# Kernel optimization log

Hardware: AMD Instinct MI355X
Metric: run time of the kernel (lower is better)

## Reference

```python
import jax, jax.numpy as jnp
import numpy as np

INPUT_SIZE = 512
HIDDEN_SIZE = 512
BATCH = 128
SEQ_LEN = 512


def setup_inputs() -> dict:
    key = jax.random.key(0)
    k_xs, k_wih, k_whh, k_b, k_bn = jax.random.split(key, 5)
    lim = 1.0 / np.sqrt(HIDDEN_SIZE)  # equinox GRUCell init: U(-1/sqrt(H), 1/sqrt(H))
    xs = jax.random.normal(k_xs, (BATCH, SEQ_LEN, INPUT_SIZE), dtype=jnp.float32)
    weight_ih = jax.random.uniform(k_wih, (3 * HIDDEN_SIZE, INPUT_SIZE), minval=-lim, maxval=lim, dtype=jnp.float32)
    weight_hh = jax.random.uniform(k_whh, (3 * HIDDEN_SIZE, HIDDEN_SIZE), minval=-lim, maxval=lim, dtype=jnp.float32)
    bias = jax.random.uniform(k_b, (3 * HIDDEN_SIZE,), minval=-lim, maxval=lim, dtype=jnp.float32)
    bias_n = jax.random.uniform(k_bn, (HIDDEN_SIZE,), minval=-lim, maxval=lim, dtype=jnp.float32)
    return {"xs": xs, "weight_ih": weight_ih, "weight_hh": weight_hh, "bias": bias, "bias_n": bias_n}


def _gru_scan(xs, weight_ih, weight_hh, bias, bias_n):
    # xs: [B, T, I]. Precompute all input-side gates in one big GEMM: [B, T, 3H]
    igates_all = jnp.einsum('bti,gi->btg', xs, weight_ih) + bias
    B = xs.shape[0]
    H = weight_hh.shape[1]

    def step(h, ig_t):  # h: [B, H], ig_t: [B, 3H]
        hg = h @ weight_hh.T  # [B, 3H]
        ir, iz, in_ = jnp.split(ig_t, 3, axis=-1)
        hr, hz, hn = jnp.split(hg, 3, axis=-1)
        r = jax.nn.sigmoid(ir + hr)
        z = jax.nn.sigmoid(iz + hz)
        n = jnp.tanh(in_ + r * (hn + bias_n))
        h_new = n + z * (h - n)  # equinox GRUCell: new + inp*(hidden - new)
        return h_new, None

    init = jnp.zeros((B, H), dtype=xs.dtype)
    final_state, _ = jax.lax.scan(step, init, jnp.swapaxes(igates_all, 0, 1))  # scan over T
    return final_state  # [B, H]


def reference(xs, weight_ih, weight_hh, bias, bias_n):
    return _gru_scan(xs, weight_ih, weight_hh, bias, bias_n)
```

## Files before the change

kernel.cpp:

```cpp
#include <hip/hip_runtime.h>
#include <hip/hip_bf16.h>
#include <stdint.h>


static constexpr int INPUT = 512;
static constexpr int HID   = 512;
static constexpr int NB    = 128;
static constexpr int TLEN  = 512;
static constexpr int BGRPS = 8;
static constexpr int UGRPS = 32;

typedef __attribute__((ext_vector_type(4))) float f32x4;
typedef __attribute__((ext_vector_type(8))) short s16x8;

static __device__ __forceinline__ unsigned short f2bf(float f) {
  unsigned u = __builtin_bit_cast(unsigned, f);
  u += 0x7FFFu + ((u >> 16) & 1u);
  return (unsigned short)(u >> 16);
}

static __device__ __forceinline__ s16x8 cvt8(const float* p) {
  f32x4 a = *(const f32x4*)p;
  f32x4 b = *(const f32x4*)(p + 4);
  s16x8 r;
  r[0] = (short)f2bf(a[0]); r[1] = (short)f2bf(a[1]);
  r[2] = (short)f2bf(a[2]); r[3] = (short)f2bf(a[3]);
  r[4] = (short)f2bf(b[0]); r[5] = (short)f2bf(b[1]);
  r[6] = (short)f2bf(b[2]); r[7] = (short)f2bf(b[3]);
  return r;
}

__global__ __launch_bounds__(192, 2) void gru_fused(
    const float* __restrict__ xs, const float* __restrict__ wih,
    const float* __restrict__ whh, const float* __restrict__ bias,
    const float* __restrict__ bias_n, float* __restrict__ out,
    unsigned short* __restrict__ hbuf, unsigned int* __restrict__ flags)
{
  const int wg   = blockIdx.x;
  const int bgrp = wg & 7;
  const int ugrp = wg >> 3;
  const int b0   = bgrp * 16;
  const int u0   = ugrp * 16;
  const int tid  = threadIdx.x;
  const int g    = tid >> 6;
  const int lane = tid & 63;
  const int ln   = lane & 15;
  const int kg   = lane >> 4;

  const int rowW = g * HID + u0 + ln;
  s16x8 wa[16], wb[16];
#pragma unroll
  for (int ks = 0; ks < 16; ++ks) {
    const int k = ks * 32 + kg * 8;
    wa[ks] = cvt8(wih + (size_t)rowW * INPUT + k);
    wb[ks] = cvt8(whh + (size_t)rowW * HID + k);
  }
  const float bv = bias[rowW];
  const float bn = bias_n[u0 + ln];

  const float* xrow = xs + (size_t)(b0 + ln) * TLEN * INPUT + kg * 8;
  const int hoff = (b0 + ln) * HID + kg * 8;

  __shared__ float xch[2][4][16][16];

  float hold[4] = {0.f, 0.f, 0.f, 0.f};

  f32x4 acc_a = {bv, bv, bv, bv};
#pragma unroll
  for (int ks = 0; ks < 16; ++ks) {
    s16x8 xa = cvt8(xrow + ks * 32);
    acc_a = __builtin_amdgcn_mfma_f32_16x16x32_bf16(xa, wa[ks], acc_a, 0, 0, 0);
  }

  for (int t = 0; t < TLEN; ++t) {
    if (t > 0) {
      const unsigned* fp = &flags[bgrp * UGRPS + (lane & 31)];
      unsigned fv;
      do {
        fv = __hip_atomic_load(fp, __ATOMIC_RELAXED, __HIP_MEMORY_SCOPE_AGENT);
      } while (~__ballot(fv >= (unsigned)t));
      __builtin_amdgcn_sched_barrier(0);
    }

    const unsigned long long* hb =
        (const unsigned long long*)(hbuf + (size_t)(t & 1) * (NB * HID) + hoff);
    unsigned long long q0[16], q1[16];
#pragma unroll
    for (int ks = 0; ks < 16; ++ks) {
      q0[ks] = __hip_atomic_load(hb + ks * 8,     __ATOMIC_RELAXED, __HIP_MEMORY_SCOPE_AGENT);
      q1[ks] = __hip_atomic_load(hb + ks * 8 + 1, __ATOMIC_RELAXED, __HIP_MEMORY_SCOPE_AGENT);
    }

    f32x4 acc_b0 = {0.f, 0.f, 0.f, 0.f}, acc_b1 = {0.f, 0.f, 0.f, 0.f};
#pragma unroll
    for (int ks = 0; ks < 16; ks += 2) {
      union { unsigned long long q[2]; s16x8 s; } ua, ub;
      ua.q[0] = q0[ks];     ua.q[1] = q1[ks];
      ub.q[0] = q0[ks + 1]; ub.q[1] = q1[ks + 1];
      acc_b0 = __builtin_amdgcn_mfma_f32_16x16x32_bf16(ua.s, wb[ks],     acc_b0, 0, 0, 0);
      acc_b1 = __builtin_amdgcn_mfma_f32_16x16x32_bf16(ub.s, wb[ks + 1], acc_b1, 0, 0, 0);
    }
    f32x4 acc_b = acc_b0 + acc_b1;

    float (*xc)[16][16] = xch[t & 1];
    if (g == 0)      { f32x4 s = acc_a + acc_b; *(f32x4*)&xc[0][ln][kg * 4] = s; }
    else if (g == 1) { f32x4 s = acc_a + acc_b; *(f32x4*)&xc[1][ln][kg * 4] = s; }
    else             { *(f32x4*)&xc[2][ln][kg * 4] = acc_a;
                       *(f32x4*)&xc[3][ln][kg * 4] = acc_b; }
    __syncthreads();
    f32x4 Sr  = *(const f32x4*)&xc[0][ln][kg * 4];
    f32x4 Sz  = *(const f32x4*)&xc[1][ln][kg * 4];
    f32x4 Snx = *(const f32x4*)&xc[2][ln][kg * 4];
    f32x4 Snh = *(const f32x4*)&xc[3][ln][kg * 4];

    float hnew[4];
#pragma unroll
    for (int i = 0; i < 4; ++i) {
      float r = 1.f / (1.f + __expf(-Sr[i]));
      float z = 1.f / (1.f + __expf(-Sz[i]));
      float pre = Snx[i] + r * (Snh[i] + bn);
      float e = __expf(2.f * pre);
      float n = 1.f - 2.f / (e + 1.f);
      hnew[i] = n + z * (hold[i] - n);
      hold[i] = hnew[i];
    }

    if (t == TLEN - 1) {
      if (g == 0) {
#pragma unroll
        for (int i = 0; i < 4; ++i)
          out[(size_t)(b0 + kg * 4 + i) * HID + u0 + ln] = hnew[i];
      }
    } else {
      if (g == 0) {
        unsigned short* hbn = hbuf + (size_t)((t + 1) & 1) * (NB * HID);
#pragma unroll
        for (int i = 0; i < 4; ++i) {
          int v  = (int)f2bf(hnew[i]);
          int o1 = __shfl_xor(v, 1);
          unsigned int p = (unsigned int)(v & 0xffff) | ((unsigned int)(o1 & 0xffff) << 16);
          unsigned int o2 = (unsigned int)__shfl_xor((int)p, 2);
          if ((ln & 3) == 0) {
            unsigned long long q = (unsigned long long)p | ((unsigned long long)o2 << 32);
            __hip_atomic_store(
                (unsigned long long*)(hbn + (size_t)(b0 + kg * 4 + i) * HID + u0 + ln),
                q, __ATOMIC_RELAXED, __HIP_MEMORY_SCOPE_AGENT);
          }
        }
        asm volatile("s_waitcnt vmcnt(0)" ::: "memory");
        if (tid == 0)
          __hip_atomic_store(&flags[bgrp * UGRPS + ugrp], (unsigned)(t + 1),
                             __ATOMIC_RELAXED, __HIP_MEMORY_SCOPE_AGENT);
      }

      acc_a = (f32x4){bv, bv, bv, bv};
      const float* xp = xrow + (size_t)(t + 1) * INPUT;
#pragma unroll
      for (int ks = 0; ks < 16; ++ks) {
        s16x8 xa = cvt8(xp + ks * 32);
        acc_a = __builtin_amdgcn_mfma_f32_16x16x32_bf16(xa, wa[ks], acc_a, 0, 0, 0);
      }
    }
  }
}

extern "C" void kernel_launch(void* const* d_in, const int* in_sizes, int n_in,
                              void* d_out, int out_size, void* d_ws, size_t ws_size,
                              hipStream_t stream) {
  const float* xs     = (const float*)d_in[0];
  const float* wih    = (const float*)d_in[1];
  const float* whh    = (const float*)d_in[2];
  const float* bias   = (const float*)d_in[3];
  const float* bias_n = (const float*)d_in[4];
  float* out = (float*)d_out;

  const size_t hbuf_bytes = (size_t)2 * NB * HID * sizeof(unsigned short);
  const size_t flg_bytes  = (size_t)BGRPS * UGRPS * sizeof(unsigned int);
  unsigned short* hbuf  = (unsigned short*)d_ws;
  unsigned int*   flags = (unsigned int*)((char*)d_ws + hbuf_bytes);

  hipMemsetAsync(d_ws, 0, hbuf_bytes + flg_bytes, stream);

  gru_fused<<<dim3(BGRPS * UGRPS), dim3(192), 0, stream>>>(
      xs, wih, whh, bias, bias_n, out, hbuf, flags);
}
```

Before: 3.553 ms.

## Use XCD-local L2-coherent loads when a batch group shares one XCD

At startup every workgroup records its XCC_ID, then checks whether all 32 workgroups of its batch group sit on the same XCD. If they do, the per-step flag polling and hidden-state exchange use plain sc0 loads and non-atomic stores, which are coherent at the XCD-local L2, in place of device-scope atomics, and the hidden-state read becomes sixteen dwordx4 loads. The bf16 conversion in cvt8 also switches to the packed hardware instruction, which changes rounding only if it differs from the old manual round-to-nearest-even. Correctness depends on the dispatch placement and on L2 coherence assumptions, and the fast path only runs when the groups land on one XCD.

```diff
diff --git a/kernel.cpp b/kernel.cpp
--- a/kernel.cpp
+++ b/kernel.cpp
@@ -12,6 +12,7 @@
 
 typedef __attribute__((ext_vector_type(4))) float f32x4;
 typedef __attribute__((ext_vector_type(8))) short s16x8;
+typedef __attribute__((ext_vector_type(4))) int   i32x4;
 
 static __device__ __forceinline__ unsigned short f2bf(float f) {
   unsigned u = __builtin_bit_cast(unsigned, f);
@@ -22,19 +23,22 @@
 static __device__ __forceinline__ s16x8 cvt8(const float* p) {
   f32x4 a = *(const f32x4*)p;
   f32x4 b = *(const f32x4*)(p + 4);
-  s16x8 r;
-  r[0] = (short)f2bf(a[0]); r[1] = (short)f2bf(a[1]);
-  r[2] = (short)f2bf(a[2]); r[3] = (short)f2bf(a[3]);
-  r[4] = (short)f2bf(b[0]); r[5] = (short)f2bf(b[1]);
-  r[6] = (short)f2bf(b[2]); r[7] = (short)f2bf(b[3]);
-  return r;
+  unsigned r0, r1, r2, r3;
+  asm("v_cvt_pk_bf16_f32 %0, %1, %2" : "=v"(r0) : "v"(a[0]), "v"(a[1]));
+  asm("v_cvt_pk_bf16_f32 %0, %1, %2" : "=v"(r1) : "v"(a[2]), "v"(a[3]));
+  asm("v_cvt_pk_bf16_f32 %0, %1, %2" : "=v"(r2) : "v"(b[0]), "v"(b[1]));
+  asm("v_cvt_pk_bf16_f32 %0, %1, %2" : "=v"(r3) : "v"(b[2]), "v"(b[3]));
+  union { unsigned u[4]; s16x8 s; } r;
+  r.u[0] = r0; r.u[1] = r1; r.u[2] = r2; r.u[3] = r3;
+  return r.s;
 }
 
 __global__ __launch_bounds__(192, 2) void gru_fused(
     const float* __restrict__ xs, const float* __restrict__ wih,
     const float* __restrict__ whh, const float* __restrict__ bias,
     const float* __restrict__ bias_n, float* __restrict__ out,
-    unsigned short* __restrict__ hbuf, unsigned int* __restrict__ flags)
+    unsigned short* __restrict__ hbuf, unsigned int* __restrict__ flags,
+    unsigned int* __restrict__ xcdmap)
 {
   const int wg   = blockIdx.x;
   const int bgrp = wg & 7;
@@ -47,6 +51,12 @@
   const int ln   = lane & 15;
   const int kg   = lane >> 4;
 
+  if (tid == 0) {
+    unsigned x;
+    asm volatile("s_getreg_b32 %0, hwreg(HW_REG_XCC_ID)" : "=s"(x));
+    __hip_atomic_store(&xcdmap[wg], x | 0x100u, __ATOMIC_RELAXED, __HIP_MEMORY_SCOPE_AGENT);
+  }
+
   const int rowW = g * HID + u0 + ln;
   s16x8 wa[16], wb[16];
 #pragma unroll
@@ -58,10 +68,22 @@
   const float bv = bias[rowW];
   const float bn = bias_n[u0 + ln];
 
+  __shared__ int fast_sh;
+  __shared__ float xch[2][4][16][16];
+  if (tid < 32) {
+    unsigned v;
+    do {
+      v = __hip_atomic_load(&xcdmap[bgrp + 8 * tid], __ATOMIC_RELAXED, __HIP_MEMORY_SCOPE_AGENT);
+    } while (v == 0);
+    unsigned v0 = (unsigned)__shfl((int)v, 0);
+    unsigned long long bal = __ballot(v == v0);
+    if (tid == 0) fast_sh = ((bal & 0xFFFFFFFFull) == 0xFFFFFFFFull) ? 1 : 0;
+  }
+  __syncthreads();
+  const bool fast = (fast_sh != 0);
+
   const float* xrow = xs + (size_t)(b0 + ln) * TLEN * INPUT + kg * 8;
   const int hoff = (b0 + ln) * HID + kg * 8;
-
-  __shared__ float xch[2][4][16][16];
 
   float hold[4] = {0.f, 0.f, 0.f, 0.f};
 
@@ -76,29 +98,71 @@
     if (t > 0) {
       const unsigned* fp = &flags[bgrp * UGRPS + (lane & 31)];
       unsigned fv;
-      do {
-        fv = __hip_atomic_load(fp, __ATOMIC_RELAXED, __HIP_MEMORY_SCOPE_AGENT);
-      } while (~__ballot(fv >= (unsigned)t));
+      if (fast) {
+        do {
+          asm volatile("global_load_dword %0, %1, off sc0\n\t"
+                       "s_waitcnt vmcnt(0)"
+                       : "=&v"(fv) : "v"(fp) : "memory");
+        } while (~__ballot(fv >= (unsigned)t));
+      } else {
+        do {
+          fv = __hip_atomic_load(fp, __ATOMIC_RELAXED, __HIP_MEMORY_SCOPE_AGENT);
+        } while (~__ballot(fv >= (unsigned)t));
+      }
       __builtin_amdgcn_sched_barrier(0);
     }
 
-    const unsigned long long* hb =
-        (const unsigned long long*)(hbuf + (size_t)(t & 1) * (NB * HID) + hoff);
-    unsigned long long q0[16], q1[16];
-#pragma unroll
-    for (int ks = 0; ks < 16; ++ks) {
-      q0[ks] = __hip_atomic_load(hb + ks * 8,     __ATOMIC_RELAXED, __HIP_MEMORY_SCOPE_AGENT);
-      q1[ks] = __hip_atomic_load(hb + ks * 8 + 1, __ATOMIC_RELAXED, __HIP_MEMORY_SCOPE_AGENT);
+    s16x8 hu[16];
+    if (fast) {
+      const char* hb = (const char*)(hbuf + (size_t)(t & 1) * (NB * HID) + hoff);
+      i32x4 h0,h1,h2,h3,h4,h5,h6,h7,h8,h9,h10,h11,h12,h13,h14,h15;
+      asm volatile(
+        "global_load_dwordx4 %0,  %16, off sc0\n\t"
+        "global_load_dwordx4 %1,  %16, off offset:64 sc0\n\t"
+        "global_load_dwordx4 %2,  %16, off offset:128 sc0\n\t"
+        "global_load_dwordx4 %3,  %16, off offset:192 sc0\n\t"
+        "global_load_dwordx4 %4,  %16, off offset:256 sc0\n\t"
+        "global_load_dwordx4 %5,  %16, off offset:320 sc0\n\t"
+        "global_load_dwordx4 %6,  %16, off offset:384 sc0\n\t"
+        "global_load_dwordx4 %7,  %16, off offset:448 sc0\n\t"
+        "global_load_dwordx4 %8,  %16, off offset:512 sc0\n\t"
+        "global_load_dwordx4 %9,  %16, off offset:576 sc0\n\t"
+        "global_load_dwordx4 %10, %16, off offset:640 sc0\n\t"
+        "global_load_dwordx4 %11, %16, off offset:704 sc0\n\t"
+        "global_load_dwordx4 %12, %16, off offset:768 sc0\n\t"
+        "global_load_dwordx4 %13, %16, off offset:832 sc0\n\t"
+        "global_load_dwordx4 %14, %16, off offset:896 sc0\n\t"
+        "global_load_dwordx4 %15, %16, off offset:960 sc0"
+        : "=&v"(h0),"=&v"(h1),"=&v"(h2),"=&v"(h3),"=&v"(h4),"=&v"(h5),"=&v"(h6),"=&v"(h7),
+          "=&v"(h8),"=&v"(h9),"=&v"(h10),"=&v"(h11),"=&v"(h12),"=&v"(h13),"=&v"(h14),"=&v"(h15)
+        : "v"(hb) : "memory");
+      asm volatile("s_waitcnt vmcnt(0)" ::: "memory");
+      __builtin_amdgcn_sched_barrier(0);
+      hu[0]=__builtin_bit_cast(s16x8,h0);   hu[1]=__builtin_bit_cast(s16x8,h1);
+      hu[2]=__builtin_bit_cast(s16x8,h2);   hu[3]=__builtin_bit_cast(s16x8,h3);
+      hu[4]=__builtin_bit_cast(s16x8,h4);   hu[5]=__builtin_bit_cast(s16x8,h5);
+      hu[6]=__builtin_bit_cast(s16x8,h6);   hu[7]=__builtin_bit_cast(s16x8,h7);
+      hu[8]=__builtin_bit_cast(s16x8,h8);   hu[9]=__builtin_bit_cast(s16x8,h9);
+      hu[10]=__builtin_bit_cast(s16x8,h10); hu[11]=__builtin_bit_cast(s16x8,h11);
+      hu[12]=__builtin_bit_cast(s16x8,h12); hu[13]=__builtin_bit_cast(s16x8,h13);
+      hu[14]=__builtin_bit_cast(s16x8,h14); hu[15]=__builtin_bit_cast(s16x8,h15);
+    } else {
+      const unsigned long long* hb =
+          (const unsigned long long*)(hbuf + (size_t)(t & 1) * (NB * HID) + hoff);
+#pragma unroll
+      for (int ks = 0; ks < 16; ++ks) {
+        union { unsigned long long q[2]; s16x8 s; } u;
+        u.q[0] = __hip_atomic_load(hb + ks * 8,     __ATOMIC_RELAXED, __HIP_MEMORY_SCOPE_AGENT);
+        u.q[1] = __hip_atomic_load(hb + ks * 8 + 1, __ATOMIC_RELAXED, __HIP_MEMORY_SCOPE_AGENT);
+        hu[ks] = u.s;
+      }
     }
 
     f32x4 acc_b0 = {0.f, 0.f, 0.f, 0.f}, acc_b1 = {0.f, 0.f, 0.f, 0.f};
 #pragma unroll
     for (int ks = 0; ks < 16; ks += 2) {
-      union { unsigned long long q[2]; s16x8 s; } ua, ub;
-      ua.q[0] = q0[ks];     ua.q[1] = q1[ks];
-      ub.q[0] = q0[ks + 1]; ub.q[1] = q1[ks + 1];
-      acc_b0 = __builtin_amdgcn_mfma_f32_16x16x32_bf16(ua.s, wb[ks],     acc_b0, 0, 0, 0);
-      acc_b1 = __builtin_amdgcn_mfma_f32_16x16x32_bf16(ub.s, wb[ks + 1], acc_b1, 0, 0, 0);
+      acc_b0 = __builtin_amdgcn_mfma_f32_16x16x32_bf16(hu[ks],     wb[ks],     acc_b0, 0, 0, 0);
+      acc_b1 = __builtin_amdgcn_mfma_f32_16x16x32_bf16(hu[ks + 1], wb[ks + 1], acc_b1, 0, 0, 0);
     }
     f32x4 acc_b = acc_b0 + acc_b1;
 
@@ -142,15 +206,19 @@
           unsigned int o2 = (unsigned int)__shfl_xor((int)p, 2);
           if ((ln & 3) == 0) {
             unsigned long long q = (unsigned long long)p | ((unsigned long long)o2 << 32);
-            __hip_atomic_store(
-                (unsigned long long*)(hbn + (size_t)(b0 + kg * 4 + i) * HID + u0 + ln),
-                q, __ATOMIC_RELAXED, __HIP_MEMORY_SCOPE_AGENT);
+            unsigned long long* qa =
+                (unsigned long long*)(hbn + (size_t)(b0 + kg * 4 + i) * HID + u0 + ln);
+            if (fast) *qa = q;
+            else __hip_atomic_store(qa, q, __ATOMIC_RELAXED, __HIP_MEMORY_SCOPE_AGENT);
           }
         }
         asm volatile("s_waitcnt vmcnt(0)" ::: "memory");
-        if (tid == 0)
-          __hip_atomic_store(&flags[bgrp * UGRPS + ugrp], (unsigned)(t + 1),
-                             __ATOMIC_RELAXED, __HIP_MEMORY_SCOPE_AGENT);
+        if (tid == 0) {
+          unsigned* fw = &flags[bgrp * UGRPS + ugrp];
+          if (fast) *(volatile unsigned*)fw = (unsigned)(t + 1);
+          else __hip_atomic_store(fw, (unsigned)(t + 1),
+                                  __ATOMIC_RELAXED, __HIP_MEMORY_SCOPE_AGENT);
+        }
       }
 
       acc_a = (f32x4){bv, bv, bv, bv};
@@ -176,11 +244,13 @@
 
   const size_t hbuf_bytes = (size_t)2 * NB * HID * sizeof(unsigned short);
   const size_t flg_bytes  = (size_t)BGRPS * UGRPS * sizeof(unsigned int);
+  const size_t xcd_bytes  = (size_t)BGRPS * UGRPS * sizeof(unsigned int);
   unsigned short* hbuf  = (unsigned short*)d_ws;
   unsigned int*   flags = (unsigned int*)((char*)d_ws + hbuf_bytes);
-
-  hipMemsetAsync(d_ws, 0, hbuf_bytes + flg_bytes, stream);
+  unsigned int*   xcdm  = (unsigned int*)((char*)d_ws + hbuf_bytes + flg_bytes);
+
+  hipMemsetAsync(d_ws, 0, hbuf_bytes + flg_bytes + xcd_bytes, stream);
 
   gru_fused<<<dim3(BGRPS * UGRPS), dim3(192), 0, stream>>>(
-      xs, wih, whh, bias, bias_n, out, hbuf, flags);
-}
+      xs, wih, whh, bias, bias_n, out, hbuf, flags, xcdm);
+}
```

Result: slower. 4.285 ms (+20.6%).

## Stage x rows through swizzled LDS ring buffer with cooperative prefetch

Applied to the files above, without the earlier changes.

Replaces each wave's redundant per-timestep global load and bf16 conversion of x with a cooperative load. All 192 threads fetch the 16x512 x tile for step t+2 into registers, convert it to bf16 and store it into a triple-buffered, XOR-swizzled LDS ring. Each wave then reads its x fragments from LDS for the input-gate MFMAs. The input-gate MFMA now runs inside the timestep after the flag wait, not after publishing h. The change also uses the hardware v_cvt_pk_bf16_f32 packed conversion instead of manual rounding. This cuts global x traffic per workgroup (three waves previously loaded the same x) and hides load latency. The cost is 48KB of LDS, which may hurt the 2-blocks-per-CU occupancy, and input-gate work placed on the critical path after the wait.

```diff
diff --git a/kernel.cpp b/kernel.cpp
--- a/kernel.cpp
+++ b/kernel.cpp
@@ -9,6 +9,8 @@
 static constexpr int TLEN  = 512;
 static constexpr int BGRPS = 8;
 static constexpr int UGRPS = 32;
+static constexpr int PD    = 2;
+static constexpr int NBUF  = 3;
 
 typedef __attribute__((ext_vector_type(4))) float f32x4;
 typedef __attribute__((ext_vector_type(8))) short s16x8;
@@ -22,12 +24,28 @@
 static __device__ __forceinline__ s16x8 cvt8(const float* p) {
   f32x4 a = *(const f32x4*)p;
   f32x4 b = *(const f32x4*)(p + 4);
-  s16x8 r;
-  r[0] = (short)f2bf(a[0]); r[1] = (short)f2bf(a[1]);
-  r[2] = (short)f2bf(a[2]); r[3] = (short)f2bf(a[3]);
-  r[4] = (short)f2bf(b[0]); r[5] = (short)f2bf(b[1]);
-  r[6] = (short)f2bf(b[2]); r[7] = (short)f2bf(b[3]);
-  return r;
+  unsigned r0, r1, r2, r3;
+  asm("v_cvt_pk_bf16_f32 %0, %1, %2" : "=v"(r0) : "v"(a[0]), "v"(a[1]));
+  asm("v_cvt_pk_bf16_f32 %0, %1, %2" : "=v"(r1) : "v"(a[2]), "v"(a[3]));
+  asm("v_cvt_pk_bf16_f32 %0, %1, %2" : "=v"(r2) : "v"(b[0]), "v"(b[1]));
+  asm("v_cvt_pk_bf16_f32 %0, %1, %2" : "=v"(r3) : "v"(b[2]), "v"(b[3]));
+  union { unsigned u[4]; s16x8 s; } r;
+  r.u[0] = r0; r.u[1] = r1; r.u[2] = r2; r.u[3] = r3;
+  return r.s;
+}
+
+static __device__ __forceinline__ int tile_byte(int idx) {
+  int rw = idx >> 7, c = idx & 127;
+  return rw * 1024 + ((c * 8) ^ ((rw & 7) << 4));
+}
+
+static __device__ __forceinline__ void st_tile(char* xtb, int idx, f32x4 v) {
+  unsigned lo, hi;
+  asm("v_cvt_pk_bf16_f32 %0, %1, %2" : "=v"(lo) : "v"(v[0]), "v"(v[1]));
+  asm("v_cvt_pk_bf16_f32 %0, %1, %2" : "=v"(hi) : "v"(v[2]), "v"(v[3]));
+  union { unsigned u[2]; unsigned long long q; } r;
+  r.u[0] = lo; r.u[1] = hi;
+  *(unsigned long long*)(xtb + tile_byte(idx)) = r.q;
 }
 
 __global__ __launch_bounds__(192, 2) void gru_fused(
@@ -47,6 +65,9 @@
   const int ln   = lane & 15;
   const int kg   = lane >> 4;
 
+  __shared__ unsigned short xt[NBUF][16 * 512];
+  __shared__ float xch[2][4][16][16];
+
   const int rowW = g * HID + u0 + ln;
   s16x8 wa[16], wb[16];
 #pragma unroll
@@ -58,19 +79,25 @@
   const float bv = bias[rowW];
   const float bn = bias_n[u0 + ln];
 
-  const float* xrow = xs + (size_t)(b0 + ln) * TLEN * INPUT + kg * 8;
+  const size_t xbase = (size_t)b0 * TLEN * INPUT;
   const int hoff = (b0 + ln) * HID + kg * 8;
 
-  __shared__ float xch[2][4][16][16];
+  for (int p = 0; p < PD; ++p) {
+    char* xtb = (char*)&xt[p][0];
+#pragma unroll
+    for (int k = 0; k < 11; ++k) {
+      int idx = tid + k * 192;
+      if (idx < 2048) {
+        int rw = idx >> 7, c = idx & 127;
+        f32x4 v = *(const f32x4*)(xs + xbase + (size_t)rw * TLEN * INPUT +
+                                  (size_t)p * INPUT + c * 4);
+        st_tile(xtb, idx, v);
+      }
+    }
+  }
+  __syncthreads();
 
   float hold[4] = {0.f, 0.f, 0.f, 0.f};
-
-  f32x4 acc_a = {bv, bv, bv, bv};
-#pragma unroll
-  for (int ks = 0; ks < 16; ++ks) {
-    s16x8 xa = cvt8(xrow + ks * 32);
-    acc_a = __builtin_amdgcn_mfma_f32_16x16x32_bf16(xa, wa[ks], acc_a, 0, 0, 0);
-  }
 
   for (int t = 0; t < TLEN; ++t) {
     if (t > 0) {
@@ -91,6 +118,31 @@
       q1[ks] = __hip_atomic_load(hb + ks * 8 + 1, __ATOMIC_RELAXED, __HIP_MEMORY_SCOPE_AGENT);
     }
 
+    f32x4 xr[11];
+    const bool do_stage = (t + PD < TLEN);
+    if (do_stage) {
+#pragma unroll
+      for (int k = 0; k < 11; ++k) {
+        int idx = tid + k * 192;
+        if (idx < 2048) {
+          int rw = idx >> 7, c = idx & 127;
+          xr[k] = *(const f32x4*)(xs + xbase + (size_t)rw * TLEN * INPUT +
+                                  (size_t)(t + PD) * INPUT + c * 4);
+        }
+      }
+    }
+
+    f32x4 acc_a = {bv, bv, bv, bv};
+    {
+      const char* xtb = (const char*)&xt[t % NBUF][0];
+#pragma unroll
+      for (int ks = 0; ks < 16; ++ks) {
+        int byte = ln * 1024 + ((ks * 64 + kg * 16) ^ ((ln & 7) << 4));
+        s16x8 xa = *(const s16x8*)(xtb + byte);
+        acc_a = __builtin_amdgcn_mfma_f32_16x16x32_bf16(xa, wa[ks], acc_a, 0, 0, 0);
+      }
+    }
+
     f32x4 acc_b0 = {0.f, 0.f, 0.f, 0.f}, acc_b1 = {0.f, 0.f, 0.f, 0.f};
 #pragma unroll
     for (int ks = 0; ks < 16; ks += 2) {
@@ -107,7 +159,17 @@
     else if (g == 1) { f32x4 s = acc_a + acc_b; *(f32x4*)&xc[1][ln][kg * 4] = s; }
     else             { *(f32x4*)&xc[2][ln][kg * 4] = acc_a;
                        *(f32x4*)&xc[3][ln][kg * 4] = acc_b; }
+
+    if (do_stage) {
+      char* xtb = (char*)&xt[(t + PD) % NBUF][0];
+#pragma unroll
+      for (int k = 0; k < 11; ++k) {
+        int idx = tid + k * 192;
+        if (idx < 2048) st_tile(xtb, idx, xr[k]);
+      }
+    }
     __syncthreads();
+
     f32x4 Sr  = *(const f32x4*)&xc[0][ln][kg * 4];
     f32x4 Sz  = *(const f32x4*)&xc[1][ln][kg * 4];
     f32x4 Snx = *(const f32x4*)&xc[2][ln][kg * 4];
@@ -152,14 +214,6 @@
           __hip_atomic_store(&flags[bgrp * UGRPS + ugrp], (unsigned)(t + 1),
                              __ATOMIC_RELAXED, __HIP_MEMORY_SCOPE_AGENT);
       }
-
-      acc_a = (f32x4){bv, bv, bv, bv};
-      const float* xp = xrow + (size_t)(t + 1) * INPUT;
-#pragma unroll
-      for (int ks = 0; ks < 16; ++ks) {
-        s16x8 xa = cvt8(xp + ks * 32);
-        acc_a = __builtin_amdgcn_mfma_f32_16x16x32_bf16(xa, wa[ks], acc_a, 0, 0, 0);
-      }
     }
   }
 }
```

Result: slower. 4.912 ms (+38.2%).

## Stage hidden state in LDS via one wave; use packed bf16 convert

Applied to the files above, without the earlier changes.

Only wave 0 now polls the per-step flags and loads the 16x512 bf16 hidden-state tile from global memory into swizzled shared memory. All three waves then read their MFMA operands from LDS after a block barrier. Before, each of the three waves spun on the flags and issued its own global atomic loads. This cuts global traffic and polling by three times, at the cost of an extra __syncthreads and LDS round trip on the critical recurrent path. The f32-to-bf16 conversion also switches to the hardware packed convert instruction instead of manual rounding.

```diff
diff --git a/kernel.cpp b/kernel.cpp
--- a/kernel.cpp
+++ b/kernel.cpp
@@ -22,12 +22,14 @@
 static __device__ __forceinline__ s16x8 cvt8(const float* p) {
   f32x4 a = *(const f32x4*)p;
   f32x4 b = *(const f32x4*)(p + 4);
-  s16x8 r;
-  r[0] = (short)f2bf(a[0]); r[1] = (short)f2bf(a[1]);
-  r[2] = (short)f2bf(a[2]); r[3] = (short)f2bf(a[3]);
-  r[4] = (short)f2bf(b[0]); r[5] = (short)f2bf(b[1]);
-  r[6] = (short)f2bf(b[2]); r[7] = (short)f2bf(b[3]);
-  return r;
+  unsigned r0, r1, r2, r3;
+  asm("v_cvt_pk_bf16_f32 %0, %1, %2" : "=v"(r0) : "v"(a[0]), "v"(a[1]));
+  asm("v_cvt_pk_bf16_f32 %0, %1, %2" : "=v"(r1) : "v"(a[2]), "v"(a[3]));
+  asm("v_cvt_pk_bf16_f32 %0, %1, %2" : "=v"(r2) : "v"(b[0]), "v"(b[1]));
+  asm("v_cvt_pk_bf16_f32 %0, %1, %2" : "=v"(r3) : "v"(b[2]), "v"(b[3]));
+  union { unsigned u[4]; s16x8 s; } r;
+  r.u[0] = r0; r.u[1] = r1; r.u[2] = r2; r.u[3] = r3;
+  return r.s;
 }
 
 __global__ __launch_bounds__(192, 2) void gru_fused(
@@ -47,6 +49,9 @@
   const int ln   = lane & 15;
   const int kg   = lane >> 4;
 
+  __shared__ unsigned short hlds[16 * 512];
+  __shared__ float xch[2][4][16][16];
+
   const int rowW = g * HID + u0 + ln;
   s16x8 wa[16], wb[16];
 #pragma unroll
@@ -59,9 +64,6 @@
   const float bn = bias_n[u0 + ln];
 
   const float* xrow = xs + (size_t)(b0 + ln) * TLEN * INPUT + kg * 8;
-  const int hoff = (b0 + ln) * HID + kg * 8;
-
-  __shared__ float xch[2][4][16][16];
 
   float hold[4] = {0.f, 0.f, 0.f, 0.f};
 
@@ -73,32 +75,40 @@
   }
 
   for (int t = 0; t < TLEN; ++t) {
-    if (t > 0) {
-      const unsigned* fp = &flags[bgrp * UGRPS + (lane & 31)];
-      unsigned fv;
-      do {
-        fv = __hip_atomic_load(fp, __ATOMIC_RELAXED, __HIP_MEMORY_SCOPE_AGENT);
-      } while (~__ballot(fv >= (unsigned)t));
-      __builtin_amdgcn_sched_barrier(0);
+    if (g == 0) {
+      if (t > 0) {
+        const unsigned* fp = &flags[bgrp * UGRPS + (lane & 31)];
+        unsigned fv;
+        do {
+          fv = __hip_atomic_load(fp, __ATOMIC_RELAXED, __HIP_MEMORY_SCOPE_AGENT);
+        } while (~__ballot(fv >= (unsigned)t));
+        __builtin_amdgcn_sched_barrier(0);
+      }
+      const unsigned long long* hs =
+          (const unsigned long long*)(hbuf + (size_t)(t & 1) * (NB * HID)) +
+          (size_t)b0 * 128;
+#pragma unroll
+      for (int r = 0; r < 16; ++r) {
+        union { unsigned long long q[2]; s16x8 s; } u;
+        u.q[0] = __hip_atomic_load(hs + r * 128 + 2 * lane,
+                                   __ATOMIC_RELAXED, __HIP_MEMORY_SCOPE_AGENT);
+        u.q[1] = __hip_atomic_load(hs + r * 128 + 2 * lane + 1,
+                                   __ATOMIC_RELAXED, __HIP_MEMORY_SCOPE_AGENT);
+        int byte = r * 1024 + ((lane * 16) ^ ((r & 7) << 4));
+        *(s16x8*)((char*)hlds + byte) = u.s;
+      }
     }
-
-    const unsigned long long* hb =
-        (const unsigned long long*)(hbuf + (size_t)(t & 1) * (NB * HID) + hoff);
-    unsigned long long q0[16], q1[16];
-#pragma unroll
-    for (int ks = 0; ks < 16; ++ks) {
-      q0[ks] = __hip_atomic_load(hb + ks * 8,     __ATOMIC_RELAXED, __HIP_MEMORY_SCOPE_AGENT);
-      q1[ks] = __hip_atomic_load(hb + ks * 8 + 1, __ATOMIC_RELAXED, __HIP_MEMORY_SCOPE_AGENT);
-    }
+    __syncthreads();
 
     f32x4 acc_b0 = {0.f, 0.f, 0.f, 0.f}, acc_b1 = {0.f, 0.f, 0.f, 0.f};
 #pragma unroll
     for (int ks = 0; ks < 16; ks += 2) {
-      union { unsigned long long q[2]; s16x8 s; } ua, ub;
-      ua.q[0] = q0[ks];     ua.q[1] = q1[ks];
-      ub.q[0] = q0[ks + 1]; ub.q[1] = q1[ks + 1];
-      acc_b0 = __builtin_amdgcn_mfma_f32_16x16x32_bf16(ua.s, wb[ks],     acc_b0, 0, 0, 0);
-      acc_b1 = __builtin_amdgcn_mfma_f32_16x16x32_bf16(ub.s, wb[ks + 1], acc_b1, 0, 0, 0);
+      int byte0 = ln * 1024 + ((ks * 64 + kg * 16) ^ ((ln & 7) << 4));
+      int byte1 = ln * 1024 + (((ks + 1) * 64 + kg * 16) ^ ((ln & 7) << 4));
+      s16x8 ha = *(const s16x8*)((const char*)hlds + byte0);
+      s16x8 hbf = *(const s16x8*)((const char*)hlds + byte1);
+      acc_b0 = __builtin_amdgcn_mfma_f32_16x16x32_bf16(ha,  wb[ks],     acc_b0, 0, 0, 0);
+      acc_b1 = __builtin_amdgcn_mfma_f32_16x16x32_bf16(hbf, wb[ks + 1], acc_b1, 0, 0, 0);
     }
     f32x4 acc_b = acc_b0 + acc_b1;
 
```

After: 5.826 ms. 64.0% more time.
